# Optimization experiments

Hardware: AMD Instinct MI355X
Metric: run time of the kernel (lower is better)

The kernel has to match this reference:

```python
import jax, jax.numpy as jnp
import numpy as np

B, S, D, N_OPS = 16, 8192, 128, 4


def setup_inputs() -> dict:
    key = jax.random.key(0)
    k1, k2, k3 = jax.random.split(key, 3)
    x = jax.random.normal(k1, (B, S, D), dtype=jnp.float32)
    # candidate op parameters: 4 Linear(D, D) layers, stacked
    W = jax.random.normal(k2, (N_OPS, D, D), dtype=jnp.float32) * (1.0 / np.sqrt(D))
    b = jax.random.normal(k3, (N_OPS, D), dtype=jnp.float32) * 0.01
    # one-hot path selector buffer: weights[0] = 1.0 (as in MixModule.__init__)
    weights = jnp.zeros((N_OPS,), dtype=jnp.float32).at[0].set(1.0)
    return {"x": x, "W": W, "b": b, "weights": weights}


def reference(x, W, b, weights):
    # Faithful to the torch loop: compute EVERY candidate op(x), then the
    # weighted (one-hot) sum. outs: [B, S, n_ops, D]
    outs = jnp.einsum("bsd,ofd->bsof", x, W) + b[None, None, :, :]
    y = jnp.einsum("bsof,o->bsf", outs, weights)
    return y
```

## Files before the change

kernel.cpp:

```cpp
#include <hip/hip_runtime.h>
#include <hip/hip_bf16.h>

#define D 128
#define NOPS 4
#define BS_STRIDE 136
#define NSLAB 2

typedef __attribute__((ext_vector_type(8))) short short8;
typedef __attribute__((ext_vector_type(4))) float float4_t;

__global__ void combine_kernel(const float* __restrict__ W,
                               const float* __restrict__ b,
                               const float* __restrict__ wts,
                               __hip_bfloat16* __restrict__ Wc,
                               float* __restrict__ bc) {
    int idx = blockIdx.x * blockDim.x + threadIdx.x;
    float w0 = wts[0], w1 = wts[1], w2 = wts[2], w3 = wts[3];
    if (idx < D * D) {
        float v = w0 * W[idx] + w1 * W[D * D + idx]
                + w2 * W[2 * D * D + idx] + w3 * W[3 * D * D + idx];
        Wc[idx] = __float2bfloat16(v);
    }
    if (idx < D) {
        bc[idx] = w0 * b[idx] + w1 * b[D + idx] + w2 * b[2 * D + idx] + w3 * b[3 * D + idx];
    }
}

__device__ inline short8 cvt8_bf16(float4_t a, float4_t b) {
    union { short8 s; __hip_bfloat16 h[8]; } u;
    u.h[0] = __float2bfloat16(a[0]);
    u.h[1] = __float2bfloat16(a[1]);
    u.h[2] = __float2bfloat16(a[2]);
    u.h[3] = __float2bfloat16(a[3]);
    u.h[4] = __float2bfloat16(b[0]);
    u.h[5] = __float2bfloat16(b[1]);
    u.h[6] = __float2bfloat16(b[2]);
    u.h[7] = __float2bfloat16(b[3]);
    return u.s;
}

__global__ __launch_bounds__(256, 4) void gemm_kernel(const float* __restrict__ x,
                                                      const __hip_bfloat16* __restrict__ Wc,
                                                      const float* __restrict__ bc,
                                                      float* __restrict__ y,
                                                      int M) {
    __shared__ __align__(16) __hip_bfloat16 Bs[D * BS_STRIDE];

    const int tid  = threadIdx.x;
    const int lane = tid & 63;
    const int wave = tid >> 6;

    #pragma unroll
    for (int i = 0; i < 8; i++) {
        int c  = i * 256 + tid;
        int n  = c >> 4;
        int ko = (c & 15) << 3;
        short8 v = *(const short8*)((const short*)Wc + n * D + ko);
        *(short8*)((short*)Bs + n * BS_STRIDE + ko) = v;
    }

    const int row  = lane & 15;
    const int quad = lane >> 4;

    float4_t bias[8];
    #pragma unroll
    for (int ft = 0; ft < 8; ft++)
        bias[ft] = *(const float4_t*)(bc + ft * 16 + quad * 4);

    __syncthreads();

    if (blockIdx.x * (64 * NSLAB) >= M) return;
    const int mbase = blockIdx.x * (64 * NSLAB) + wave * 16 + row;

    #pragma unroll
    for (int s = 0; s < NSLAB; s++) {
        const int m = mbase + s * 64;

        const float* xp = x + (size_t)m * D + quad * 8;
        short8 xf[4];
        #pragma unroll
        for (int ks = 0; ks < 4; ks++) {
            float4_t a0 = __builtin_nontemporal_load((const float4_t*)(xp + ks * 32));
            float4_t a1 = __builtin_nontemporal_load((const float4_t*)(xp + ks * 32 + 4));
            xf[ks] = cvt8_bf16(a0, a1);
        }

        float4_t acc[8];
        #pragma unroll
        for (int i = 0; i < 8; i++) acc[i] = (float4_t)(0.f);

        #pragma unroll
        for (int ks = 0; ks < 4; ks++) {
            const short* bp = (const short*)Bs + ks * 32 + quad * 8;
            #pragma unroll
            for (int ft = 0; ft < 8; ft++) {
                short8 wfrag = *(const short8*)(bp + (ft * 16 + row) * BS_STRIDE);
                acc[ft] = __builtin_amdgcn_mfma_f32_16x16x32_bf16(wfrag, xf[ks], acc[ft], 0, 0, 0);
            }
        }

        float* yp = y + (size_t)m * D + quad * 4;
        #pragma unroll
        for (int ft = 0; ft < 8; ft++) {
            float4_t out;
            out[0] = acc[ft][0] + bias[ft][0];
            out[1] = acc[ft][1] + bias[ft][1];
            out[2] = acc[ft][2] + bias[ft][2];
            out[3] = acc[ft][3] + bias[ft][3];
            __builtin_nontemporal_store(out, (float4_t*)(yp + ft * 16));
        }
    }
}

extern "C" void kernel_launch(void* const* d_in, const int* in_sizes, int n_in,
                              void* d_out, int out_size, void* d_ws, size_t ws_size,
                              hipStream_t stream) {
    const float* x   = (const float*)d_in[0];
    const float* W   = (const float*)d_in[1];
    const float* b   = (const float*)d_in[2];
    const float* wts = (const float*)d_in[3];
    float* y = (float*)d_out;

    __hip_bfloat16* Wc = (__hip_bfloat16*)d_ws;
    float* bc = (float*)((char*)d_ws + D * D * sizeof(__hip_bfloat16));

    combine_kernel<<<(D * D + 255) / 256, 256, 0, stream>>>(W, b, wts, Wc, bc);

    const int M = in_sizes[0] / D;
    gemm_kernel<<<M / (64 * NSLAB), 256, 0, stream>>>(x, Wc, bc, y, M);
}
```

Before: 132.6 us.

## Split output columns across wave pairs with 512-thread blocks

Doubles the block to 512 threads, with each pair of waves sharing a 16-row slab and each wave computing half of the 128 output columns. This halves the accumulators per wave and raises the number of waves in flight to better hide the memory latency of a bandwidth-bound GEMM. Each x row is now loaded by two waves, relying on cache hits, and the x loads switch from nontemporal to normal so the second reader can hit in cache. Bias is now loaded in the epilogue instead of being held in registers.

```diff
diff --git a/kernel.cpp b/kernel.cpp
--- a/kernel.cpp
+++ b/kernel.cpp
@@ -4,7 +4,7 @@
 #define D 128
 #define NOPS 4
 #define BS_STRIDE 136
-#define NSLAB 2
+#define ROWS_PER_BLOCK 128
 
 typedef __attribute__((ext_vector_type(8))) short short8;
 typedef __attribute__((ext_vector_type(4))) float float4_t;
@@ -39,75 +39,73 @@
     return u.s;
 }
 
-__global__ __launch_bounds__(256, 4) void gemm_kernel(const float* __restrict__ x,
+__global__ __launch_bounds__(512, 8) void gemm_kernel(const float* __restrict__ x,
                                                       const __hip_bfloat16* __restrict__ Wc,
                                                       const float* __restrict__ bc,
                                                       float* __restrict__ y,
                                                       int M) {
     __shared__ __align__(16) __hip_bfloat16 Bs[D * BS_STRIDE];
 
-    const int tid  = threadIdx.x;
-    const int lane = tid & 63;
-    const int wave = tid >> 6;
+    const int tid   = threadIdx.x;
+    const int lane  = tid & 63;
+    const int wave  = tid >> 6;
+    const int wslab = wave >> 1;
+    const int whalf = wave & 1;
 
     #pragma unroll
-    for (int i = 0; i < 8; i++) {
-        int c  = i * 256 + tid;
+    for (int i = 0; i < 4; i++) {
+        int c  = i * 512 + tid;
         int n  = c >> 4;
         int ko = (c & 15) << 3;
         short8 v = *(const short8*)((const short*)Wc + n * D + ko);
         *(short8*)((short*)Bs + n * BS_STRIDE + ko) = v;
     }
+    __syncthreads();
 
     const int row  = lane & 15;
     const int quad = lane >> 4;
 
-    float4_t bias[8];
-    #pragma unroll
-    for (int ft = 0; ft < 8; ft++)
-        bias[ft] = *(const float4_t*)(bc + ft * 16 + quad * 4);
+    const int mbase = blockIdx.x * ROWS_PER_BLOCK + wslab * 16 + row;
+    if (mbase >= M) return;
 
-    __syncthreads();
-
-    if (blockIdx.x * (64 * NSLAB) >= M) return;
-    const int mbase = blockIdx.x * (64 * NSLAB) + wave * 16 + row;
+    const short* bp0 = (const short*)Bs + (whalf * 64 + row) * BS_STRIDE + quad * 8;
 
     #pragma unroll
-    for (int s = 0; s < NSLAB; s++) {
+    for (int s = 0; s < 2; s++) {
         const int m = mbase + s * 64;
 
         const float* xp = x + (size_t)m * D + quad * 8;
         short8 xf[4];
         #pragma unroll
         for (int ks = 0; ks < 4; ks++) {
-            float4_t a0 = __builtin_nontemporal_load((const float4_t*)(xp + ks * 32));
-            float4_t a1 = __builtin_nontemporal_load((const float4_t*)(xp + ks * 32 + 4));
+            float4_t a0 = *(const float4_t*)(xp + ks * 32);
+            float4_t a1 = *(const float4_t*)(xp + ks * 32 + 4);
             xf[ks] = cvt8_bf16(a0, a1);
         }
 
-        float4_t acc[8];
+        float4_t acc[4];
         #pragma unroll
-        for (int i = 0; i < 8; i++) acc[i] = (float4_t)(0.f);
+        for (int i = 0; i < 4; i++) acc[i] = (float4_t)(0.f);
 
         #pragma unroll
         for (int ks = 0; ks < 4; ks++) {
-            const short* bp = (const short*)Bs + ks * 32 + quad * 8;
             #pragma unroll
-            for (int ft = 0; ft < 8; ft++) {
-                short8 wfrag = *(const short8*)(bp + (ft * 16 + row) * BS_STRIDE);
-                acc[ft] = __builtin_amdgcn_mfma_f32_16x16x32_bf16(wfrag, xf[ks], acc[ft], 0, 0, 0);
+            for (int f = 0; f < 4; f++) {
+                short8 wfrag = *(const short8*)(bp0 + f * 16 * BS_STRIDE + ks * 32);
+                acc[f] = __builtin_amdgcn_mfma_f32_16x16x32_bf16(wfrag, xf[ks], acc[f], 0, 0, 0);
             }
         }
 
-        float* yp = y + (size_t)m * D + quad * 4;
+        float* yp = y + (size_t)m * D + whalf * 64 + quad * 4;
         #pragma unroll
-        for (int ft = 0; ft < 8; ft++) {
+        for (int f = 0; f < 4; f++) {
+            float4_t bias = *(const float4_t*)(bc + whalf * 64 + f * 16 + quad * 4);
             float4_t out;
-            out[0] = acc[ft][0] + bias[ft][0];
-            out[1] = acc[ft][1] + bias[ft][1];
-            out[2] = acc[ft][2] + bias[ft][2];
-            out[3] = acc[ft][3] + bias[ft][3];
-            __builtin_nontemporal_store(out, (float4_t*)(yp + ft * 16));
+            out[0] = acc[f][0] + bias[0];
+            out[1] = acc[f][1] + bias[1];
+            out[2] = acc[f][2] + bias[2];
+            out[3] = acc[f][3] + bias[3];
+            __builtin_nontemporal_store(out, (float4_t*)(yp + f * 16));
         }
     }
 }
@@ -127,5 +125,5 @@
     combine_kernel<<<(D * D + 255) / 256, 256, 0, stream>>>(W, b, wts, Wc, bc);
 
     const int M = in_sizes[0] / D;
-    gemm_kernel<<<M / (64 * NSLAB), 256, 0, stream>>>(x, Wc, bc, y, M);
+    gemm_kernel<<<M / ROWS_PER_BLOCK, 512, 0, stream>>>(x, Wc, bc, y, M);
 }
```

Result: faster. 128.0 us (-3.5%).
